# Optimization experiments

Measured on AMD Instinct MI355X. Metric: run time of the kernel, lower is better.

Reference implementation:

```python
import jax, jax.numpy as jnp
import numpy as np

B, S, H, E, D, K = 2, 2048, 2048, 8, 2048, 2


def setup_inputs() -> dict:
    key = jax.random.key(0)
    ks = jax.random.split(key, 4)
    # lecun_normal-style scaling: std = 1/sqrt(fan_in)
    return {
        "x": jax.random.normal(ks[0], (B, S, H), jnp.float32),
        "router_w": jax.random.normal(ks[1], (H, E), jnp.float32) / np.sqrt(H).astype(np.float32),
        "router_b": jnp.zeros((E,), jnp.float32),
        "expert_w": jax.random.normal(ks[2], (E, H, D), jnp.float32) / np.sqrt(H).astype(np.float32),
        "expert_b": jnp.zeros((E, D), jnp.float32),
        "out_w": jax.random.normal(ks[3], (D, D), jnp.float32) / np.sqrt(D).astype(np.float32),
        "out_b": jnp.zeros((D,), jnp.float32),
    }


def reference(x, router_w, router_b, expert_w, expert_b, out_w, out_b):
    num_experts = expert_w.shape[0]
    # Router: logits -> softmax -> top-2 -> renormalize
    router_logits = jnp.einsum("bsh,he->bse", x, router_w) + router_b
    router_probs = jax.nn.softmax(router_logits, axis=-1)
    top_k_probs, top_k_indices = jax.lax.top_k(router_probs, K)  # [B,S,K]
    top_k_probs = top_k_probs / jnp.sum(top_k_probs, axis=-1, keepdims=True)
    # Per-expert gate weight: sum of top-k probs routed to that expert. [B,S,E]
    onehot = jax.nn.one_hot(top_k_indices, num_experts, dtype=x.dtype)  # [B,S,K,E]
    gates = jnp.einsum("bsk,bske->bse", top_k_probs, onehot)
    # Dense per-expert GEMM + gelu (mask-and-multiply MoE; gate==0 kills unrouted tokens)
    expert_out = jax.nn.gelu(jnp.einsum("bsh,ehd->ebsd", x, expert_w) + expert_b[:, None, None, :])
    combined = jnp.einsum("bse,ebsd->bsd", gates, expert_out)
    # Output projection
    return jnp.einsum("bsd,df->bsf", combined, out_w) + out_b
```

## Files before the change

kernel.cpp:

```cpp
#include <hip/hip_runtime.h>
#include <stdint.h>

#define H_DIM 2048
#define E_NUM 8
#define D_DIM 2048
#define NTOK 4096
#define BM 128
#define BN 128
#define BK 32

typedef __bf16 bf16x8 __attribute__((ext_vector_type(8)));
typedef float f32x4 __attribute__((ext_vector_type(4)));

__device__ __forceinline__ unsigned short f2bf(float f) {
    union { float f; uint32_t u; } c; c.f = f;
    uint32_t r = (c.u + 0x7FFFu + ((c.u >> 16) & 1u)) >> 16;
    return (unsigned short)r;
}
__device__ __forceinline__ float bf2f(unsigned short h) {
    union { float f; uint32_t u; } c; c.u = ((uint32_t)h) << 16;
    return c.f;
}

__device__ __forceinline__ void gl_lds16(const unsigned short* g, unsigned short* l) {
    __builtin_amdgcn_global_load_lds(
        (const __attribute__((address_space(1))) unsigned int*)g,
        (__attribute__((address_space(3))) unsigned int*)l, 16, 0, 0);
}

__global__ __launch_bounds__(256) void router_cvt_kernel(
    const float* __restrict__ x, const float* __restrict__ rw,
    const float* __restrict__ rb, int* __restrict__ counts,
    uint32_t* __restrict__ tok, float* __restrict__ gate,
    unsigned short* __restrict__ xb) {
    int t = (blockIdx.x * 256 + threadIdx.x) >> 6;
    int lane = threadIdx.x & 63;
    const float* xr = x + (size_t)t * H_DIM;
    unsigned short* xo = xb + (size_t)t * H_DIM;
    float p[E_NUM];
#pragma unroll
    for (int e = 0; e < E_NUM; e++) p[e] = 0.f;
#pragma unroll
    for (int pass = 0; pass < H_DIM / 256; pass++) {
        int h = pass * 256 + lane * 4;
        float4 v = *(const float4*)(xr + h);
        ushort4 o;
        o.x = f2bf(v.x); o.y = f2bf(v.y); o.z = f2bf(v.z); o.w = f2bf(v.w);
        *(ushort4*)(xo + h) = o;
        const float* r0 = rw + (size_t)h * E_NUM;
#pragma unroll
        for (int e = 0; e < E_NUM; e++)
            p[e] += v.x * r0[e] + v.y * r0[e + 8] + v.z * r0[e + 16] + v.w * r0[e + 24];
    }
#pragma unroll
    for (int e = 0; e < E_NUM; e++) {
#pragma unroll
        for (int off = 1; off < 64; off <<= 1) p[e] += __shfl_xor(p[e], off, 64);
    }
    if (lane == 0) {
        float l[E_NUM];
#pragma unroll
        for (int e = 0; e < E_NUM; e++) l[e] = p[e] + rb[e];
        int e0 = 0;
#pragma unroll
        for (int e = 1; e < E_NUM; e++) if (l[e] > l[e0]) e0 = e;
        int e1 = (e0 == 0) ? 1 : 0;
#pragma unroll
        for (int e = 0; e < E_NUM; e++) if (e != e0 && l[e] > l[e1]) e1 = e;
        float g0 = 1.f / (1.f + __expf(l[e1] - l[e0]));
        float g1 = 1.f - g0;
        int p0 = atomicAdd(&counts[e0], 1);
        tok[e0 * NTOK + p0] = (uint32_t)t;
        gate[e0 * NTOK + p0] = g0;
        int p1 = atomicAdd(&counts[e1], 1);
        tok[e1 * NTOK + p1] = (uint32_t)t | (1u << 16);
        gate[e1 * NTOK + p1] = g1;
    }
}

__global__ __launch_bounds__(256) void transpose_cvt_kernel(
    const float* __restrict__ src, unsigned short* __restrict__ dst,
    int K_, int N_) {
    __shared__ unsigned short tile[64][72];
    size_t moff = (size_t)blockIdx.z * (size_t)K_ * N_;
    const float* s = src + moff;
    unsigned short* d = dst + moff;
    int k0 = blockIdx.y * 64, n0 = blockIdx.x * 64;
    int r = threadIdx.x >> 4;
    int c = (threadIdx.x & 15) * 4;
#pragma unroll
    for (int p = 0; p < 4; p++) {
        int k = p * 16 + r;
        float4 v = *(const float4*)(s + (size_t)(k0 + k) * N_ + n0 + c);
        tile[k][c + 0] = f2bf(v.x);
        tile[k][c + 1] = f2bf(v.y);
        tile[k][c + 2] = f2bf(v.z);
        tile[k][c + 3] = f2bf(v.w);
    }
    __syncthreads();
#pragma unroll
    for (int p = 0; p < 4; p++) {
        int n = p * 16 + r;
        ushort4 o;
        o.x = tile[c + 0][n];
        o.y = tile[c + 1][n];
        o.z = tile[c + 2][n];
        o.w = tile[c + 3][n];
        *(ushort4*)(d + (size_t)(n0 + n) * K_ + k0 + c) = o;
    }
}

__global__ __launch_bounds__(256) void expert_gemm_kernel(
    const unsigned short* __restrict__ xb,
    const unsigned short* __restrict__ ewT,
    const float* __restrict__ eb,
    const int* __restrict__ counts,
    const uint32_t* __restrict__ tok,
    const float* __restrict__ gate,
    unsigned short* __restrict__ Y)
{
    int e = blockIdx.z;
    int cnt = counts[e];
    int m0 = blockIdx.y * BM;
    if (m0 >= cnt) return;
    int n0 = blockIdx.x * BN;

    __shared__ unsigned short As[BM][BK];
    __shared__ unsigned short Bs[BN][BK];
    __shared__ uint32_t tok_s[BM];
    __shared__ float gate_s[BM];

    int tid = threadIdx.x;
    if (tid < BM) {
        int idx = m0 + tid;
        uint32_t tk = 0; float g = 0.f;
        if (idx < cnt) { tk = tok[e * NTOK + idx]; g = gate[e * NTOK + idx]; }
        tok_s[tid] = tk; gate_s[tid] = g;
    }
    __syncthreads();

    int lane = tid & 63;
    int wave = tid >> 6;
    int sr = lane >> 2;
    int sc = (lane & 3) * 8;
    int r0 = wave * 32 + sr;
    int r1 = wave * 32 + 16 + sr;
    const unsigned short* agp0 = xb + (size_t)(tok_s[r0] & 0xFFFFu) * H_DIM + sc;
    const unsigned short* agp1 = xb + (size_t)(tok_s[r1] & 0xFFFFu) * H_DIM + sc;
    const unsigned short* bbase = ewT + (size_t)e * D_DIM * H_DIM;
    const unsigned short* bgp0 = bbase + (size_t)(n0 + r0) * H_DIM + sc;
    const unsigned short* bgp1 = bbase + (size_t)(n0 + r1) * H_DIM + sc;
    unsigned short* la0 = &As[wave * 32][0];
    unsigned short* la1 = &As[wave * 32 + 16][0];
    unsigned short* lb0 = &Bs[wave * 32][0];
    unsigned short* lb1 = &Bs[wave * 32 + 16][0];

    int wm = (wave >> 1) * 64;
    int wn = (wave & 1) * 64;
    int row16 = lane & 15;
    int quad = lane >> 4;
    int k8 = quad * 8;

    f32x4 acc[4][4];
#pragma unroll
    for (int i = 0; i < 4; i++)
#pragma unroll
        for (int j = 0; j < 4; j++) acc[i][j] = (f32x4)(0.f);

    for (int kk = 0; kk < H_DIM; kk += BK) {
        __syncthreads();
        gl_lds16(agp0 + kk, la0);
        gl_lds16(agp1 + kk, la1);
        gl_lds16(bgp0 + kk, lb0);
        gl_lds16(bgp1 + kk, lb1);
        __syncthreads();
        bf16x8 af[4], bff[4];
#pragma unroll
        for (int i = 0; i < 4; i++)
            af[i] = *(const bf16x8*)&As[wm + i * 16 + row16][k8];
#pragma unroll
        for (int j = 0; j < 4; j++)
            bff[j] = *(const bf16x8*)&Bs[wn + j * 16 + row16][k8];
#pragma unroll
        for (int i = 0; i < 4; i++)
#pragma unroll
            for (int j = 0; j < 4; j++)
                acc[i][j] = __builtin_amdgcn_mfma_f32_16x16x32_bf16(
                    af[i], bff[j], acc[i][j], 0, 0, 0);
    }

#pragma unroll
    for (int i = 0; i < 4; i++) {
        int rbase = wm + i * 16 + quad * 4;
#pragma unroll
        for (int j = 0; j < 4; j++) {
            int n = n0 + wn + j * 16 + row16;
            float bias = eb[e * D_DIM + n];
#pragma unroll
            for (int r = 0; r < 4; r++) {
                int lrow = rbase + r;
                if (m0 + lrow < cnt) {
                    uint32_t tk = tok_s[lrow];
                    float g = gate_s[lrow];
                    float v = acc[i][j][r] + bias;
                    float q = 0.7978845608028654f * (v + 0.044715f * v * v * v);
                    float gl = v / (1.f + __expf(-2.f * q));
                    int token = tk & 0xFFFF;
                    int slot = (tk >> 16) & 1;
                    Y[((size_t)token * 2 + slot) * D_DIM + n] = f2bf(g * gl);
                }
            }
        }
    }
}

__global__ __launch_bounds__(256) void combine_kernel(
    const unsigned short* __restrict__ Y, unsigned short* __restrict__ comb) {
    int i = blockIdx.x * 256 + threadIdx.x;
    int t = i >> 8;
    int dc = (i & 255) * 8;
    uint4 u0 = *(const uint4*)(Y + (size_t)t * 2 * D_DIM + dc);
    uint4 u1 = *(const uint4*)(Y + ((size_t)t * 2 + 1) * D_DIM + dc);
    uint4 o;
    uint32_t* po = (uint32_t*)&o;
    const uint32_t* p0 = (const uint32_t*)&u0;
    const uint32_t* p1 = (const uint32_t*)&u1;
#pragma unroll
    for (int k = 0; k < 4; k++) {
        uint32_t a = p0[k], b = p1[k];
        float s0 = bf2f((unsigned short)(a & 0xFFFF)) + bf2f((unsigned short)(b & 0xFFFF));
        float s1 = bf2f((unsigned short)(a >> 16)) + bf2f((unsigned short)(b >> 16));
        po[k] = (uint32_t)f2bf(s0) | ((uint32_t)f2bf(s1) << 16);
    }
    *(uint4*)(comb + (size_t)t * D_DIM + dc) = o;
}

__global__ __launch_bounds__(256) void out_gemm_kernel(
    const unsigned short* __restrict__ comb,
    const unsigned short* __restrict__ owT,
    const float* __restrict__ ob,
    float* __restrict__ out) {
    int m0 = blockIdx.y * BM, n0 = blockIdx.x * BN;
    __shared__ unsigned short As[BM][BK];
    __shared__ unsigned short Bs[BN][BK];
    int tid = threadIdx.x;
    int lane = tid & 63;
    int wave = tid >> 6;
    int sr = lane >> 2;
    int sc = (lane & 3) * 8;
    int r0 = wave * 32 + sr;
    int r1 = wave * 32 + 16 + sr;
    const unsigned short* agp0 = comb + (size_t)(m0 + r0) * D_DIM + sc;
    const unsigned short* agp1 = comb + (size_t)(m0 + r1) * D_DIM + sc;
    const unsigned short* bgp0 = owT + (size_t)(n0 + r0) * D_DIM + sc;
    const unsigned short* bgp1 = owT + (size_t)(n0 + r1) * D_DIM + sc;
    unsigned short* la0 = &As[wave * 32][0];
    unsigned short* la1 = &As[wave * 32 + 16][0];
    unsigned short* lb0 = &Bs[wave * 32][0];
    unsigned short* lb1 = &Bs[wave * 32 + 16][0];

    int wm = (wave >> 1) * 64;
    int wn = (wave & 1) * 64;
    int row16 = lane & 15;
    int quad = lane >> 4;
    int k8 = quad * 8;

    f32x4 acc[4][4];
#pragma unroll
    for (int i = 0; i < 4; i++)
#pragma unroll
        for (int j = 0; j < 4; j++) acc[i][j] = (f32x4)(0.f);

    for (int kk = 0; kk < D_DIM; kk += BK) {
        __syncthreads();
        gl_lds16(agp0 + kk, la0);
        gl_lds16(agp1 + kk, la1);
        gl_lds16(bgp0 + kk, lb0);
        gl_lds16(bgp1 + kk, lb1);
        __syncthreads();
        bf16x8 af[4], bff[4];
#pragma unroll
        for (int i = 0; i < 4; i++)
            af[i] = *(const bf16x8*)&As[wm + i * 16 + row16][k8];
#pragma unroll
        for (int j = 0; j < 4; j++)
            bff[j] = *(const bf16x8*)&Bs[wn + j * 16 + row16][k8];
#pragma unroll
        for (int i = 0; i < 4; i++)
#pragma unroll
            for (int j = 0; j < 4; j++)
                acc[i][j] = __builtin_amdgcn_mfma_f32_16x16x32_bf16(
                    af[i], bff[j], acc[i][j], 0, 0, 0);
    }

#pragma unroll
    for (int i = 0; i < 4; i++) {
        int rbase = m0 + wm + i * 16 + quad * 4;
#pragma unroll
        for (int j = 0; j < 4; j++) {
            int n = n0 + wn + j * 16 + row16;
            float bias = ob[n];
#pragma unroll
            for (int r = 0; r < 4; r++) {
                out[(size_t)(rbase + r) * D_DIM + n] = acc[i][j][r] + bias;
            }
        }
    }
}

extern "C" void kernel_launch(void* const* d_in, const int* in_sizes, int n_in,
                              void* d_out, int out_size, void* d_ws, size_t ws_size,
                              hipStream_t stream) {
    const float* x        = (const float*)d_in[0];
    const float* router_w = (const float*)d_in[1];
    const float* router_b = (const float*)d_in[2];
    const float* expert_w = (const float*)d_in[3];
    const float* expert_b = (const float*)d_in[4];
    const float* out_w    = (const float*)d_in[5];
    const float* out_b    = (const float*)d_in[6];
    float* out = (float*)d_out;

    char* w = (char*)d_ws;
    int* counts = (int*)w;
    uint32_t* tok = (uint32_t*)(w + 256);
    float* gate = (float*)(w + 256 + E_NUM * NTOK * 4);
    size_t off = 256 + (size_t)2 * E_NUM * NTOK * 4;
    unsigned short* xb = (unsigned short*)(w + off);
    off += (size_t)NTOK * H_DIM * 2;
    unsigned short* ewT = (unsigned short*)(w + off);
    off += (size_t)E_NUM * H_DIM * D_DIM * 2;
    unsigned short* owT = (unsigned short*)(w + off);
    off += (size_t)D_DIM * D_DIM * 2;
    unsigned short* Y = (unsigned short*)(w + off);
    off += (size_t)NTOK * 2 * D_DIM * 2;
    unsigned short* comb = (unsigned short*)(w + off);

    hipMemsetAsync(d_ws, 0, 256, stream);
    router_cvt_kernel<<<NTOK / 4, 256, 0, stream>>>(x, router_w, router_b,
                                                    counts, tok, gate, xb);
    transpose_cvt_kernel<<<dim3(32, 32, 8), 256, 0, stream>>>(expert_w, ewT, H_DIM, D_DIM);
    transpose_cvt_kernel<<<dim3(32, 32, 1), 256, 0, stream>>>(out_w, owT, D_DIM, D_DIM);
    expert_gemm_kernel<<<dim3(16, 32, 8), 256, 0, stream>>>(xb, ewT, expert_b, counts, tok, gate, Y);
    combine_kernel<<<NTOK * D_DIM / 8 / 256, 256, 0, stream>>>(Y, comb);
    out_gemm_kernel<<<dim3(16, 32), 256, 0, stream>>>(comb, owT, out_b, out);
}
```

Before: 534.7 us.

## XOR-swizzle LDS tiles in GEMMs and merge weight transpose launches

Applies an XOR swizzle to the 16-byte chunk position, both when global data is written into the As/Bs shared tiles and when MFMA fragments are read back, to avoid LDS bank conflicts in the expert and output GEMMs. The two transpose/convert launches are merged into one 9-slice launch. Each block now covers 128 k-values and writes 16-byte transposed rows instead of ushort4. The workspace header grows from 256 to 1024 bytes, which relies on owT sitting directly after ewT in the workspace.

```diff
diff --git a/kernel.cpp b/kernel.cpp
--- a/kernel.cpp
+++ b/kernel.cpp
@@ -79,34 +79,32 @@
 }
 
 __global__ __launch_bounds__(256) void transpose_cvt_kernel(
-    const float* __restrict__ src, unsigned short* __restrict__ dst,
-    int K_, int N_) {
-    __shared__ unsigned short tile[64][72];
-    size_t moff = (size_t)blockIdx.z * (size_t)K_ * N_;
-    const float* s = src + moff;
-    unsigned short* d = dst + moff;
-    int k0 = blockIdx.y * 64, n0 = blockIdx.x * 64;
-    int r = threadIdx.x >> 4;
-    int c = (threadIdx.x & 15) * 4;
+    const float* __restrict__ ew, const float* __restrict__ ow,
+    unsigned short* __restrict__ ewT) {
+    __shared__ unsigned short t[64][136];
+    int z = blockIdx.z;
+    const float* s = (z < 8) ? (ew + (size_t)z * H_DIM * D_DIM) : ow;
+    unsigned short* d = ewT + (size_t)z * H_DIM * D_DIM;
+    int n0 = blockIdx.x * 64, k0 = blockIdx.y * 128;
+    int tid = threadIdx.x;
+    int rr = tid >> 4;
+    int c4 = (tid & 15) * 4;
+#pragma unroll
+    for (int p = 0; p < 8; p++) {
+        int k = p * 16 + rr;
+        float4 v = *(const float4*)(s + (size_t)(k0 + k) * D_DIM + n0 + c4);
+        t[c4 + 0][k] = f2bf(v.x);
+        t[c4 + 1][k] = f2bf(v.y);
+        t[c4 + 2][k] = f2bf(v.z);
+        t[c4 + 3][k] = f2bf(v.w);
+    }
+    __syncthreads();
+    int kc = (tid & 15) * 8;
 #pragma unroll
     for (int p = 0; p < 4; p++) {
-        int k = p * 16 + r;
-        float4 v = *(const float4*)(s + (size_t)(k0 + k) * N_ + n0 + c);
-        tile[k][c + 0] = f2bf(v.x);
-        tile[k][c + 1] = f2bf(v.y);
-        tile[k][c + 2] = f2bf(v.z);
-        tile[k][c + 3] = f2bf(v.w);
-    }
-    __syncthreads();
-#pragma unroll
-    for (int p = 0; p < 4; p++) {
-        int n = p * 16 + r;
-        ushort4 o;
-        o.x = tile[c + 0][n];
-        o.y = tile[c + 1][n];
-        o.z = tile[c + 2][n];
-        o.w = tile[c + 3][n];
-        *(ushort4*)(d + (size_t)(n0 + n) * K_ + k0 + c) = o;
+        int n = p * 16 + rr;
+        uint4 v = *(const uint4*)&t[n][kc];
+        *(uint4*)(d + (size_t)(n0 + n) * H_DIM + k0 + kc) = v;
     }
 }
 
@@ -142,7 +140,7 @@
     int lane = tid & 63;
     int wave = tid >> 6;
     int sr = lane >> 2;
-    int sc = (lane & 3) * 8;
+    int sc = ((lane & 3) ^ ((lane >> 3) & 3)) * 8;
     int r0 = wave * 32 + sr;
     int r1 = wave * 32 + 16 + sr;
     const unsigned short* agp0 = xb + (size_t)(tok_s[r0] & 0xFFFFu) * H_DIM + sc;
@@ -159,7 +157,15 @@
     int wn = (wave & 1) * 64;
     int row16 = lane & 15;
     int quad = lane >> 4;
-    int k8 = quad * 8;
+    int slot = (quad ^ ((row16 >> 1) & 3)) * 16;
+    int aoffA[4], aoffB[4];
+#pragma unroll
+    for (int i = 0; i < 4; i++) {
+        aoffA[i] = (wm + i * 16 + row16) * (BK * 2) + slot;
+        aoffB[i] = (wn + i * 16 + row16) * (BK * 2) + slot;
+    }
+    const char* pA = (const char*)&As[0][0];
+    const char* pB = (const char*)&Bs[0][0];
 
     f32x4 acc[4][4];
 #pragma unroll
@@ -176,11 +182,10 @@
         __syncthreads();
         bf16x8 af[4], bff[4];
 #pragma unroll
-        for (int i = 0; i < 4; i++)
-            af[i] = *(const bf16x8*)&As[wm + i * 16 + row16][k8];
-#pragma unroll
-        for (int j = 0; j < 4; j++)
-            bff[j] = *(const bf16x8*)&Bs[wn + j * 16 + row16][k8];
+        for (int i = 0; i < 4; i++) {
+            af[i] = *(const bf16x8*)(pA + aoffA[i]);
+            bff[i] = *(const bf16x8*)(pB + aoffB[i]);
+        }
 #pragma unroll
         for (int i = 0; i < 4; i++)
 #pragma unroll
@@ -206,8 +211,8 @@
                     float q = 0.7978845608028654f * (v + 0.044715f * v * v * v);
                     float gl = v / (1.f + __expf(-2.f * q));
                     int token = tk & 0xFFFF;
-                    int slot = (tk >> 16) & 1;
-                    Y[((size_t)token * 2 + slot) * D_DIM + n] = f2bf(g * gl);
+                    int slot2 = (tk >> 16) & 1;
+                    Y[((size_t)token * 2 + slot2) * D_DIM + n] = f2bf(g * gl);
                 }
             }
         }
@@ -247,7 +252,7 @@
     int lane = tid & 63;
     int wave = tid >> 6;
     int sr = lane >> 2;
-    int sc = (lane & 3) * 8;
+    int sc = ((lane & 3) ^ ((lane >> 3) & 3)) * 8;
     int r0 = wave * 32 + sr;
     int r1 = wave * 32 + 16 + sr;
     const unsigned short* agp0 = comb + (size_t)(m0 + r0) * D_DIM + sc;
@@ -263,7 +268,15 @@
     int wn = (wave & 1) * 64;
     int row16 = lane & 15;
     int quad = lane >> 4;
-    int k8 = quad * 8;
+    int slot = (quad ^ ((row16 >> 1) & 3)) * 16;
+    int aoffA[4], aoffB[4];
+#pragma unroll
+    for (int i = 0; i < 4; i++) {
+        aoffA[i] = (wm + i * 16 + row16) * (BK * 2) + slot;
+        aoffB[i] = (wn + i * 16 + row16) * (BK * 2) + slot;
+    }
+    const char* pA = (const char*)&As[0][0];
+    const char* pB = (const char*)&Bs[0][0];
 
     f32x4 acc[4][4];
 #pragma unroll
@@ -280,11 +293,10 @@
         __syncthreads();
         bf16x8 af[4], bff[4];
 #pragma unroll
-        for (int i = 0; i < 4; i++)
-            af[i] = *(const bf16x8*)&As[wm + i * 16 + row16][k8];
-#pragma unroll
-        for (int j = 0; j < 4; j++)
-            bff[j] = *(const bf16x8*)&Bs[wn + j * 16 + row16][k8];
+        for (int i = 0; i < 4; i++) {
+            af[i] = *(const bf16x8*)(pA + aoffA[i]);
+            bff[i] = *(const bf16x8*)(pB + aoffB[i]);
+        }
 #pragma unroll
         for (int i = 0; i < 4; i++)
 #pragma unroll
@@ -322,9 +334,9 @@
 
     char* w = (char*)d_ws;
     int* counts = (int*)w;
-    uint32_t* tok = (uint32_t*)(w + 256);
-    float* gate = (float*)(w + 256 + E_NUM * NTOK * 4);
-    size_t off = 256 + (size_t)2 * E_NUM * NTOK * 4;
+    uint32_t* tok = (uint32_t*)(w + 1024);
+    float* gate = (float*)(w + 1024 + E_NUM * NTOK * 4);
+    size_t off = 1024 + (size_t)2 * E_NUM * NTOK * 4;
     unsigned short* xb = (unsigned short*)(w + off);
     off += (size_t)NTOK * H_DIM * 2;
     unsigned short* ewT = (unsigned short*)(w + off);
@@ -335,12 +347,12 @@
     off += (size_t)NTOK * 2 * D_DIM * 2;
     unsigned short* comb = (unsigned short*)(w + off);
 
-    hipMemsetAsync(d_ws, 0, 256, stream);
+    hipMemsetAsync(d_ws, 0, 1024, stream);
     router_cvt_kernel<<<NTOK / 4, 256, 0, stream>>>(x, router_w, router_b,
                                                     counts, tok, gate, xb);
-    transpose_cvt_kernel<<<dim3(32, 32, 8), 256, 0, stream>>>(expert_w, ewT, H_DIM, D_DIM);
-    transpose_cvt_kernel<<<dim3(32, 32, 1), 256, 0, stream>>>(out_w, owT, D_DIM, D_DIM);
-    expert_gemm_kernel<<<dim3(16, 32, 8), 256, 0, stream>>>(xb, ewT, expert_b, counts, tok, gate, Y);
+    transpose_cvt_kernel<<<dim3(32, 16, 9), 256, 0, stream>>>(expert_w, out_w, ewT);
+    expert_gemm_kernel<<<dim3(16, 32, 8), 256, 0, stream>>>(
+        xb, ewT, expert_b, counts, tok, gate, Y);
     combine_kernel<<<NTOK * D_DIM / 8 / 256, 256, 0, stream>>>(Y, comb);
     out_gemm_kernel<<<dim3(16, 32), 256, 0, stream>>>(comb, owT, out_b, out);
 }
```

After: 529.2 us. About the same (-1.0%).
